# Performance work log

Measured on AMD Instinct MI355X. Metric: run time of the kernel, lower is better.

## Reference

```python
import jax, jax.numpy as jnp
import numpy as np

B, N, M = 8, 4096, 77
Q_DIM, CTX_DIM = 1024, 768
H, D = 16, 64
INNER = H * D  # 1024


def setup_inputs() -> dict:
    key = jax.random.key(0)
    ks = jax.random.split(key, 7)
    x = jax.random.normal(ks[0], (B, N, Q_DIM), dtype=jnp.float32)
    context = jax.random.normal(ks[1], (B, M, CTX_DIM), dtype=jnp.float32)
    # Linear weights stored as [in, out] so y = x @ W (no bias for q/k/v).
    Wq = jax.random.normal(ks[2], (Q_DIM, INNER), dtype=jnp.float32) * (Q_DIM ** -0.5)
    Wk = jax.random.normal(ks[3], (CTX_DIM, INNER), dtype=jnp.float32) * (CTX_DIM ** -0.5)
    Wv = jax.random.normal(ks[4], (CTX_DIM, INNER), dtype=jnp.float32) * (CTX_DIM ** -0.5)
    Wo = jax.random.normal(ks[5], (INNER, Q_DIM), dtype=jnp.float32) * (INNER ** -0.5)
    bo = jax.random.normal(ks[6], (Q_DIM,), dtype=jnp.float32) * 0.01
    return {"x": x, "context": context, "Wq": Wq, "Wk": Wk, "Wv": Wv, "Wo": Wo, "bo": bo}


def reference(x, context, Wq, Wk, Wv, Wo, bo):
    scale = D ** -0.5
    # Project and split heads: [B, S, H*D] -> [B, H, S, D]
    def heads(t):
        b, s, _ = t.shape
        return t.reshape(b, s, H, D).transpose(0, 2, 1, 3)
    q = heads(x @ Wq)        # [B, H, N, D]
    k = heads(context @ Wk)  # [B, H, M, D]
    v = heads(context @ Wv)  # [B, H, M, D]
    scores = jnp.einsum('bhid,bhjd->bhij', q, k) * scale  # [B, H, N, M]
    attn = jax.nn.softmax(scores, axis=-1)
    out = jnp.einsum('bhij,bhjd->bhid', attn, v)          # [B, H, N, D]
    out = out.transpose(0, 2, 1, 3).reshape(x.shape[0], x.shape[1], INNER)
    return out @ Wo + bo  # dropout p=0.0 -> identity
```

## Files before the change

kernel.cpp:

```cpp
#include <hip/hip_runtime.h>
#include <hip/hip_bf16.h>

typedef _Float16 f16x8 __attribute__((ext_vector_type(8)));
typedef float f32x4 __attribute__((ext_vector_type(4)));

#define MFMA16(a, b, c) __builtin_amdgcn_mfma_f32_16x16x32_f16(a, b, c, 0, 0, 0)

__device__ __forceinline__ void load_lds16(const void* g, void* l) {
  __builtin_amdgcn_global_load_lds(
      (__attribute__((address_space(1))) void*)g,
      (__attribute__((address_space(3))) void*)l, 16, 0, 0);
}

__global__ __launch_bounds__(256) void k_prep(const float* __restrict__ x,
                                              const float* __restrict__ ctx,
                                              const float* __restrict__ Wq,
                                              const float* __restrict__ Wk,
                                              const float* __restrict__ Wv,
                                              const float* __restrict__ Wo,
                                              _Float16* __restrict__ xh,
                                              _Float16* __restrict__ ctxh,
                                              _Float16* __restrict__ Wqt,
                                              _Float16* __restrict__ Wkt,
                                              _Float16* __restrict__ Wvt,
                                              _Float16* __restrict__ Wot,
                                              _Float16* __restrict__ Vtg) {
  __shared__ float tile[64][65];
  const int b = blockIdx.x, t = threadIdx.x;

  if (b < 4096) {
    for (int i = b * 256 + t; i < 4194304; i += 4096 * 256) {
      const float4* p = (const float4*)(x + (size_t)i * 8);
      float4 a = p[0], c = p[1];
      f16x8 v = {(_Float16)a.x, (_Float16)a.y, (_Float16)a.z, (_Float16)a.w,
                 (_Float16)c.x, (_Float16)c.y, (_Float16)c.z, (_Float16)c.w};
      *(f16x8*)(xh + (size_t)i * 8) = v;
    }
    return;
  }
  if (b < 4327) {
    int i = (b - 4096) * 256 + t;
    const float4* p = (const float4*)(ctx + (size_t)i * 8);
    float4 a = p[0], c = p[1];
    f16x8 v = {(_Float16)a.x, (_Float16)a.y, (_Float16)a.z, (_Float16)a.w,
               (_Float16)c.x, (_Float16)c.y, (_Float16)c.z, (_Float16)c.w};
    *(f16x8*)(ctxh + (size_t)i * 8) = v;
    return;
  }
  if (b >= 5223) {
    int i = (b - 5223) * 256 + t;
    ((f16x8*)Vtg)[i] = f16x8{};
    return;
  }
  const float* tin;
  _Float16* tout;
  int TK, TN, i;
  if (b < 4583)      { tin = Wq; tout = Wqt; TK = 1024; TN = 1024; i = b - 4327; }
  else if (b < 4775) { tin = Wk; tout = Wkt; TK = 768;  TN = 1024; i = b - 4583; }
  else if (b < 4967) { tin = Wv; tout = Wvt; TK = 768;  TN = 1024; i = b - 4775; }
  else               { tin = Wo; tout = Wot; TK = 1024; TN = 1024; i = b - 4967; }
  int n0 = (i & 15) * 64, k0 = (i >> 4) * 64;
  {
    int nn = t & 63, kb = t >> 6;
#pragma unroll
    for (int s = 0; s < 16; ++s) {
      int kk = kb + s * 4;
      tile[kk][nn] = tin[(size_t)(k0 + kk) * TN + n0 + nn];
    }
  }
  __syncthreads();
  {
    int kk = t & 63, nb = t >> 6;
#pragma unroll
    for (int s = 0; s < 16; ++s) {
      int nn = nb + s * 4;
      tout[(size_t)(n0 + nn) * TK + k0 + kk] = (_Float16)tile[kk][nn];
    }
  }
}

__global__ __launch_bounds__(64) void k_kvproj(const _Float16* __restrict__ ctxh,
                                               const _Float16* __restrict__ Wkt,
                                               const _Float16* __restrict__ Wvt,
                                               _Float16* __restrict__ Kg,
                                               _Float16* __restrict__ Vtg) {
  int mt = blockIdx.x, nt = blockIdx.y;
  int lane = threadIdx.x;
  int l15 = lane & 15, lhi = lane >> 4;
  int arow = mt * 16 + l15;
  if (arow > 615) arow = 615;
  const _Float16* ap = ctxh + (size_t)arow * 768 + lhi * 8;
  const _Float16* kp = Wkt + (size_t)(nt * 16 + l15) * 768 + lhi * 8;
  const _Float16* vp = Wvt + (size_t)(nt * 16 + l15) * 768 + lhi * 8;
  f32x4 ak = {0.f, 0.f, 0.f, 0.f}, av = {0.f, 0.f, 0.f, 0.f};
#pragma unroll 4
  for (int ks = 0; ks < 24; ++ks) {
    f16x8 a = *(const f16x8*)(ap + ks * 32);
    f16x8 bk = *(const f16x8*)(kp + ks * 32);
    f16x8 bv = *(const f16x8*)(vp + ks * 32);
    ak = MFMA16(a, bk, ak);
    av = MFMA16(a, bv, av);
  }
  int n = nt * 16 + l15, h = n >> 6, d = n & 63;
#pragma unroll
  for (int j = 0; j < 4; ++j) {
    int gm = mt * 16 + lhi * 4 + j;
    if (gm < 616) {
      int b = gm / 77, m = gm - b * 77;
      Kg[((size_t)(b * 16 + h) * 77 + m) * 64 + d] = (_Float16)ak[j];
      Vtg[((size_t)(b * 16 + h) * 64 + d) * 128 + m] = (_Float16)av[j];
    }
  }
}

template <int MODE>
__global__ __launch_bounds__(512, 2) void k_gemm9(const _Float16* __restrict__ A,
                                                  const _Float16* __restrict__ Bt,
                                                  void* __restrict__ Cout,
                                                  const float* __restrict__ bias,
                                                  const _Float16* __restrict__ Kg,
                                                  const _Float16* __restrict__ Vtg,
                                                  int M, int N, int K) {
  __shared__ __align__(16) char lds[MODE == 0 ? 163840 : 131072];
  const int t = threadIdx.x, wid = t >> 6, lane = t & 63;
  const int wr = wid >> 2, wc = wid & 3;
  const int l15 = lane & 15, lhi = lane >> 4;

  int nwg = gridDim.x, bid = blockIdx.x;
  int wg = ((nwg & 7) == 0) ? ((bid & 7) * (nwg >> 3) + (bid >> 3)) : bid;
  const int nTN = N >> 8;
  const int tm = wg / nTN, tn = wg % nTN;

  const _Float16* Ag = A + (size_t)tm * 256 * K;
  const _Float16* Bg = Bt + (size_t)tn * 256 * K;
  const size_t stg = (size_t)(wid * 8 + (lane >> 3)) * K +
                     (size_t)(((lane & 7) ^ ((lane >> 3) & 7)) * 8);
  const int dstg = wid * 1024;

  const int x7 = l15 & 7;
  const int cs0 = (lhi ^ x7) << 4;
  const int cs1 = ((4 + lhi) ^ x7) << 4;
  const int aoff = wr * 16384 + l15 * 128;
  const int boff = 32768 + wc * 8192 + l15 * 128;

  f32x4 acc[8][4];
#pragma unroll
  for (int i = 0; i < 8; ++i)
#pragma unroll
    for (int j = 0; j < 4; ++j) acc[i][j] = f32x4{0.f, 0.f, 0.f, 0.f};
  f16x8 a0k0[4], a0k1[4], a1k0[4], a1k1[4];
  f16x8 b00[2], b01[2], b10[2], b11[2];

#define STG_A(T, RB) load_lds16(Ag + stg + (size_t)(RB) * K + (T) * 64, \
                                lds + ((T) & 1) * 65536 + (RB) * 128 + dstg)
#define STG_B(T, RB) load_lds16(Bg + stg + (size_t)(RB) * K + (T) * 64, \
                                lds + ((T) & 1) * 65536 + 32768 + (RB) * 128 + dstg)
#define STG_TILE(T) { STG_A(T, 0); STG_A(T, 64); STG_A(T, 128); STG_A(T, 192);  \
                      STG_B(T, 0); STG_B(T, 64); STG_B(T, 128); STG_B(T, 192); }
#define RDA(DST, BUF, MH, CS) { const int p_ = (BUF) * 65536 + aoff + (MH) * 8192; \
    _Pragma("unroll") for (int mf = 0; mf < 4; ++mf)                               \
      DST[mf] = *(const f16x8*)&lds[p_ + mf * 2048 + (CS)]; }
#define RDB(DST, BUF, NH, CS) { const int q_ = (BUF) * 65536 + boff + (NH) * 4096; \
    _Pragma("unroll") for (int nf = 0; nf < 2; ++nf)                               \
      DST[nf] = *(const f16x8*)&lds[q_ + nf * 2048 + (CS)]; }
#define MMC(MH, NH, AR, BR) { __builtin_amdgcn_s_setprio(1);                       \
    _Pragma("unroll") for (int mf = 0; mf < 4; ++mf)                               \
      _Pragma("unroll") for (int nf = 0; nf < 2; ++nf)                             \
        acc[(MH)*4+mf][(NH)*2+nf] = MFMA16(AR[mf], BR[nf],                         \
                                           acc[(MH)*4+mf][(NH)*2+nf]);             \
    __builtin_amdgcn_s_setprio(0); }
#define VM0 asm volatile("s_waitcnt vmcnt(0)" ::: "memory")
#define BAR __builtin_amdgcn_s_barrier()

#define TILE(BUF, T, STG_ON)                                                       \
  {                                                                                \
    VM0; BAR;                                                                      \
    RDA(a0k0, BUF, 0, cs0); RDB(b00, BUF, 0, cs0);                                 \
    RDB(b10, BUF, 1, cs0);                                                         \
    if (STG_ON) STG_TILE((T) + 1);                                                 \
    MMC(0, 0, a0k0, b00);                                                          \
    RDA(a1k0, BUF, 1, cs0); MMC(0, 1, a0k0, b10);                                  \
    RDA(a1k1, BUF, 1, cs1); MMC(1, 1, a1k0, b10);                                  \
    RDB(b01, BUF, 0, cs1);  MMC(1, 0, a1k0, b00);                                  \
    RDB(b11, BUF, 1, cs1);  MMC(1, 0, a1k1, b01);                                  \
    RDA(a0k1, BUF, 0, cs1); MMC(1, 1, a1k1, b11);                                  \
    MMC(0, 1, a0k1, b11);                                                          \
    MMC(0, 0, a0k1, b01);                                                          \
  }

  const int nT = K >> 6;

  STG_TILE(0);

  for (int i = 0; i < (nT >> 1) - 1; ++i) {
    TILE(0, 2 * i, true);
    TILE(1, 2 * i + 1, true);
  }
  TILE(0, nT - 2, true);
  TILE(1, nT - 1, false);

  if (MODE == 1) {
    const long rbase = (long)tm * 256 + wr * 128;
    const int cbase = tn * 256 + wc * 64;
#pragma unroll
    for (int mf = 0; mf < 8; ++mf)
#pragma unroll
      for (int nf = 0; nf < 4; ++nf) {
        int c = cbase + nf * 16 + l15;
        float bv = bias[c];
#pragma unroll
        for (int j = 0; j < 4; ++j) {
          long r = rbase + mf * 16 + lhi * 4 + j;
          ((float*)Cout)[r * N + c] = acc[mf][nf][j] + bv;
        }
      }
    return;
  }

  BAR;

  const int h = tn * 4 + wc;
  const int bh = (tm >> 4) * 16 + h;
  const _Float16* Kgp = Kg + (size_t)bh * (77 * 64);
  const _Float16* Vgp = Vtg + (size_t)bh * (64 * 128);

  const int qbase = wid * 16384;
#pragma unroll
  for (int mf = 0; mf < 8; ++mf)
#pragma unroll
    for (int nf = 0; nf < 4; ++nf)
#pragma unroll
      for (int j = 0; j < 4; ++j) {
        int row = mf * 16 + lhi * 4 + j;
        int d = nf * 16 + l15;
        int by = (row * 128 + d * 2) ^ ((row & 7) << 4);
        *(_Float16*)&lds[qbase + by] = (_Float16)acc[mf][nf][j];
      }

  const int pbase = 131072 + wid * 4096;
#pragma unroll
  for (int i = 0; i < 4; ++i)
    *(f16x8*)&lds[pbase + lane * 64 + i * 16] = f16x8{};

  f16x8 kf[5][2];
#pragma unroll
  for (int ct = 0; ct < 5; ++ct) {
    int m = ct * 16 + l15;
    kf[ct][0] = *(const f16x8*)(Kgp + m * 64 + lhi * 8);
    kf[ct][1] = *(const f16x8*)(Kgp + m * 64 + 32 + lhi * 8);
  }
  f16x8 vf[3][4];
#pragma unroll
  for (int ks = 0; ks < 3; ++ks)
#pragma unroll
    for (int dt = 0; dt < 4; ++dt) {
      int d = dt * 16 + l15;
      vf[ks][dt] = *(const f16x8*)(Vgp + d * 128 + ks * 32 + lhi * 8);
    }

  const long orow0 = (long)tm * 256 + wr * 128;
  _Float16* aOut = (_Float16*)Cout;

  for (int mf = 0; mf < 8; ++mf) {
    const int qm = qbase + mf * 2048 + l15 * 128;
    f16x8 q0 = *(const f16x8*)&lds[qm + cs0];
    f16x8 q1 = *(const f16x8*)&lds[qm + cs1];

    float e[5][4];
    float mx[4] = {-1e30f, -1e30f, -1e30f, -1e30f};
#pragma unroll
    for (int ct = 0; ct < 5; ++ct) {
      f32x4 s = {0.f, 0.f, 0.f, 0.f};
      s = MFMA16(q0, kf[ct][0], s);
      s = MFMA16(q1, kf[ct][1], s);
      bool valid = (ct * 16 + l15) < 77;
#pragma unroll
      for (int j = 0; j < 4; ++j) {
        float v = valid ? s[j] * 0.125f : -1e30f;
        e[ct][j] = v;
        mx[j] = fmaxf(mx[j], v);
      }
    }
#pragma unroll
    for (int off = 1; off < 16; off <<= 1)
#pragma unroll
      for (int j = 0; j < 4; ++j) mx[j] = fmaxf(mx[j], __shfl_xor(mx[j], off, 64));
    float sm[4] = {0.f, 0.f, 0.f, 0.f};
#pragma unroll
    for (int ct = 0; ct < 5; ++ct)
#pragma unroll
      for (int j = 0; j < 4; ++j) {
        float ev = __expf(e[ct][j] - mx[j]);
        e[ct][j] = ev;
        sm[j] += ev;
      }
#pragma unroll
    for (int off = 1; off < 16; off <<= 1)
#pragma unroll
      for (int j = 0; j < 4; ++j) sm[j] += __shfl_xor(sm[j], off, 64);
    float rs[4];
#pragma unroll
    for (int j = 0; j < 4; ++j) rs[j] = 1.0f / sm[j];

#pragma unroll
    for (int ct = 0; ct < 5; ++ct) {
      int m = ct * 16 + l15;
#pragma unroll
      for (int j = 0; j < 4; ++j) {
        int r = lhi * 4 + j;
        *(_Float16*)&lds[pbase + ((r * 256 + m * 2) ^ ((r & 7) << 4))] =
            (_Float16)(e[ct][j] * rs[j]);
      }
    }

    f32x4 o[4] = {{0.f,0.f,0.f,0.f},{0.f,0.f,0.f,0.f},{0.f,0.f,0.f,0.f},{0.f,0.f,0.f,0.f}};
#pragma unroll
    for (int ks = 0; ks < 3; ++ks) {
      int m0b = ks * 64 + lhi * 16;
      f16x8 pa = *(const f16x8*)&lds[pbase + ((l15 * 256 + m0b) ^ ((l15 & 7) << 4))];
#pragma unroll
      for (int dt = 0; dt < 4; ++dt)
        o[dt] = MFMA16(pa, vf[ks][dt], o[dt]);
    }
    _Float16* op = aOut + (size_t)(orow0 + mf * 16 + lhi * 4) * 1024 + h * 64;
#pragma unroll
    for (int dt = 0; dt < 4; ++dt)
#pragma unroll
      for (int j = 0; j < 4; ++j)
        op[(size_t)j * 1024 + dt * 16 + l15] = (_Float16)o[dt][j];
  }
#undef STG_A
#undef STG_B
#undef STG_TILE
#undef RDA
#undef RDB
#undef MMC
#undef TILE
#undef VM0
#undef BAR
}

extern "C" void kernel_launch(void* const* d_in, const int* in_sizes, int n_in,
                              void* d_out, int out_size, void* d_ws, size_t ws_size,
                              hipStream_t stream) {
  const float* x   = (const float*)d_in[0];
  const float* ctx = (const float*)d_in[1];
  const float* Wq  = (const float*)d_in[2];
  const float* Wk  = (const float*)d_in[3];
  const float* Wv  = (const float*)d_in[4];
  const float* Wo  = (const float*)d_in[5];
  const float* bo  = (const float*)d_in[6];

  char* ws = (char*)d_ws;
  _Float16* xh   = (_Float16*)(ws + 0);
  _Float16* Wqt  = (_Float16*)(ws + 67108864);
  _Float16* Wkt  = (_Float16*)(ws + 69206016);
  _Float16* Wvt  = (_Float16*)(ws + 70778880);
  _Float16* Wot  = (_Float16*)(ws + 72351744);
  _Float16* ctxh = (_Float16*)(ws + 74448896);
  _Float16* Kg   = (_Float16*)(ws + 75395072);
  _Float16* Vtg  = (_Float16*)(ws + 76656640);
  _Float16* aOut = (_Float16*)(ws + 78774272);

  k_prep<<<5735, 256, 0, stream>>>(x, ctx, Wq, Wk, Wv, Wo,
                                   xh, ctxh, Wqt, Wkt, Wvt, Wot, Vtg);
  k_kvproj<<<dim3(39, 64), 64, 0, stream>>>(ctxh, Wkt, Wvt, Kg, Vtg);
  k_gemm9<0><<<dim3(512), dim3(512), 0, stream>>>(xh, Wqt, (void*)aOut, nullptr,
                                                  Kg, Vtg, 32768, 1024, 1024);
  k_gemm9<1><<<dim3(512), dim3(512), 0, stream>>>(aOut, Wot, d_out, bo,
                                                  nullptr, nullptr, 32768, 1024, 1024);
}
```

Measured before the change: 244.1 us.

## Fuse fp32-to-fp16 conversion of x into the Q-projection GEMM A-tile loads

Removes the separate pass that converted x to fp16 in the prep kernel and instead loads fp32 x directly inside the first GEMM, converting in registers and writing fp16 into LDS. This eliminates a full write and re-read of an fp16 copy of x. In exchange, the GEMM reads fp32 A (twice the bytes per tile, repeated across N tiles), uses extra registers for staging, and adds LDS write and waits to the pipelined loop.

```diff
diff --git a/kernel.cpp b/kernel.cpp
--- a/kernel.cpp
+++ b/kernel.cpp
@@ -12,13 +12,11 @@
       (__attribute__((address_space(3))) void*)l, 16, 0, 0);
 }
 
-__global__ __launch_bounds__(256) void k_prep(const float* __restrict__ x,
-                                              const float* __restrict__ ctx,
+__global__ __launch_bounds__(256) void k_prep(const float* __restrict__ ctx,
                                               const float* __restrict__ Wq,
                                               const float* __restrict__ Wk,
                                               const float* __restrict__ Wv,
                                               const float* __restrict__ Wo,
-                                              _Float16* __restrict__ xh,
                                               _Float16* __restrict__ ctxh,
                                               _Float16* __restrict__ Wqt,
                                               _Float16* __restrict__ Wkt,
@@ -28,18 +26,8 @@
   __shared__ float tile[64][65];
   const int b = blockIdx.x, t = threadIdx.x;
 
-  if (b < 4096) {
-    for (int i = b * 256 + t; i < 4194304; i += 4096 * 256) {
-      const float4* p = (const float4*)(x + (size_t)i * 8);
-      float4 a = p[0], c = p[1];
-      f16x8 v = {(_Float16)a.x, (_Float16)a.y, (_Float16)a.z, (_Float16)a.w,
-                 (_Float16)c.x, (_Float16)c.y, (_Float16)c.z, (_Float16)c.w};
-      *(f16x8*)(xh + (size_t)i * 8) = v;
-    }
-    return;
-  }
-  if (b < 4327) {
-    int i = (b - 4096) * 256 + t;
+  if (b < 231) {
+    int i = b * 256 + t;
     const float4* p = (const float4*)(ctx + (size_t)i * 8);
     float4 a = p[0], c = p[1];
     f16x8 v = {(_Float16)a.x, (_Float16)a.y, (_Float16)a.z, (_Float16)a.w,
@@ -47,18 +35,18 @@
     *(f16x8*)(ctxh + (size_t)i * 8) = v;
     return;
   }
-  if (b >= 5223) {
-    int i = (b - 5223) * 256 + t;
+  if (b >= 1127) {
+    int i = (b - 1127) * 256 + t;
     ((f16x8*)Vtg)[i] = f16x8{};
     return;
   }
   const float* tin;
   _Float16* tout;
   int TK, TN, i;
-  if (b < 4583)      { tin = Wq; tout = Wqt; TK = 1024; TN = 1024; i = b - 4327; }
-  else if (b < 4775) { tin = Wk; tout = Wkt; TK = 768;  TN = 1024; i = b - 4583; }
-  else if (b < 4967) { tin = Wv; tout = Wvt; TK = 768;  TN = 1024; i = b - 4775; }
-  else               { tin = Wo; tout = Wot; TK = 1024; TN = 1024; i = b - 4967; }
+  if (b < 487)      { tin = Wq; tout = Wqt; TK = 1024; TN = 1024; i = b - 231; }
+  else if (b < 679) { tin = Wk; tout = Wkt; TK = 768;  TN = 1024; i = b - 487; }
+  else if (b < 871) { tin = Wv; tout = Wvt; TK = 768;  TN = 1024; i = b - 679; }
+  else              { tin = Wo; tout = Wot; TK = 1024; TN = 1024; i = b - 871; }
   int n0 = (i & 15) * 64, k0 = (i >> 4) * 64;
   {
     int nn = t & 63, kb = t >> 6;
@@ -115,6 +103,7 @@
 
 template <int MODE>
 __global__ __launch_bounds__(512, 2) void k_gemm9(const _Float16* __restrict__ A,
+                                                  const float* __restrict__ Axf,
                                                   const _Float16* __restrict__ Bt,
                                                   void* __restrict__ Cout,
                                                   const float* __restrict__ bias,
@@ -136,6 +125,9 @@
   const size_t stg = (size_t)(wid * 8 + (lane >> 3)) * K +
                      (size_t)(((lane & 7) ^ ((lane >> 3) & 7)) * 8);
   const int dstg = wid * 1024;
+  const float* Axp = Axf + (size_t)(tm * 256 + wid * 8 + (lane >> 3)) * K +
+                     (size_t)(((lane & 7) ^ ((lane >> 3) & 7)) * 8);
+  const int awr = dstg + lane * 16;
 
   const int x7 = l15 & 7;
   const int cs0 = (lhi ^ x7) << 4;
@@ -150,13 +142,20 @@
     for (int j = 0; j < 4; ++j) acc[i][j] = f32x4{0.f, 0.f, 0.f, 0.f};
   f16x8 a0k0[4], a0k1[4], a1k0[4], a1k1[4];
   f16x8 b00[2], b01[2], b10[2], b11[2];
+  float4 ar0[4], ar1[4];
 
 #define STG_A(T, RB) load_lds16(Ag + stg + (size_t)(RB) * K + (T) * 64, \
                                 lds + ((T) & 1) * 65536 + (RB) * 128 + dstg)
 #define STG_B(T, RB) load_lds16(Bg + stg + (size_t)(RB) * K + (T) * 64, \
                                 lds + ((T) & 1) * 65536 + 32768 + (RB) * 128 + dstg)
-#define STG_TILE(T) { STG_A(T, 0); STG_A(T, 64); STG_A(T, 128); STG_A(T, 192);  \
-                      STG_B(T, 0); STG_B(T, 64); STG_B(T, 128); STG_B(T, 192); }
+#define LD_A32(T) { _Pragma("unroll") for (int s = 0; s < 4; ++s) {                \
+      const float* sp_ = Axp + (size_t)s * 64 * K + (T) * 64;                      \
+      ar0[s] = *(const float4*)sp_; ar1[s] = *(const float4*)(sp_ + 4); } }
+#define WR_A(T) { _Pragma("unroll") for (int s = 0; s < 4; ++s) {                  \
+      f16x8 v_ = {(_Float16)ar0[s].x, (_Float16)ar0[s].y, (_Float16)ar0[s].z,      \
+                  (_Float16)ar0[s].w, (_Float16)ar1[s].x, (_Float16)ar1[s].y,      \
+                  (_Float16)ar1[s].z, (_Float16)ar1[s].w};                         \
+      *(f16x8*)&lds[((T) & 1) * 65536 + s * 8192 + awr] = v_; } }
 #define RDA(DST, BUF, MH, CS) { const int p_ = (BUF) * 65536 + aoff + (MH) * 8192; \
     _Pragma("unroll") for (int mf = 0; mf < 4; ++mf)                               \
       DST[mf] = *(const f16x8*)&lds[p_ + mf * 2048 + (CS)]; }
@@ -170,14 +169,17 @@
                                            acc[(MH)*4+mf][(NH)*2+nf]);             \
     __builtin_amdgcn_s_setprio(0); }
 #define VM0 asm volatile("s_waitcnt vmcnt(0)" ::: "memory")
+#define VMLG0 asm volatile("s_waitcnt vmcnt(0) lgkmcnt(0)" ::: "memory")
 #define BAR __builtin_amdgcn_s_barrier()
 
-#define TILE(BUF, T, STG_ON)                                                       \
+#define TILE1(BUF, T, STG_ON)                                                      \
   {                                                                                \
     VM0; BAR;                                                                      \
     RDA(a0k0, BUF, 0, cs0); RDB(b00, BUF, 0, cs0);                                 \
     RDB(b10, BUF, 1, cs0);                                                         \
-    if (STG_ON) STG_TILE((T) + 1);                                                 \
+    if (STG_ON) { STG_A((T) + 1, 0); STG_A((T) + 1, 64); STG_A((T) + 1, 128);      \
+                  STG_A((T) + 1, 192); STG_B((T) + 1, 0); STG_B((T) + 1, 64);      \
+                  STG_B((T) + 1, 128); STG_B((T) + 1, 192); }                      \
     MMC(0, 0, a0k0, b00);                                                          \
     RDA(a1k0, BUF, 1, cs0); MMC(0, 1, a0k0, b10);                                  \
     RDA(a1k1, BUF, 1, cs1); MMC(1, 1, a1k0, b10);                                  \
@@ -187,17 +189,48 @@
     MMC(0, 1, a0k1, b11);                                                          \
     MMC(0, 0, a0k1, b01);                                                          \
   }
+#define TILE0(BUF, T, STG_ON)                                                      \
+  {                                                                                \
+    VMLG0; BAR;                                                                    \
+    RDA(a0k0, BUF, 0, cs0); RDB(b00, BUF, 0, cs0);                                 \
+    RDB(b10, BUF, 1, cs0);                                                         \
+    if (STG_ON) { LD_A32((T) + 1); STG_B((T) + 1, 0); STG_B((T) + 1, 64);          \
+                  STG_B((T) + 1, 128); STG_B((T) + 1, 192); }                      \
+    MMC(0, 0, a0k0, b00);                                                          \
+    RDA(a1k0, BUF, 1, cs0); MMC(0, 1, a0k0, b10);                                  \
+    RDA(a1k1, BUF, 1, cs1); MMC(1, 1, a1k0, b10);                                  \
+    RDB(b01, BUF, 0, cs1);  MMC(1, 0, a1k0, b00);                                  \
+    RDB(b11, BUF, 1, cs1);  MMC(1, 0, a1k1, b01);                                  \
+    RDA(a0k1, BUF, 0, cs1); MMC(1, 1, a1k1, b11);                                  \
+    if (STG_ON) WR_A((T) + 1);                                                     \
+    MMC(0, 1, a0k1, b11);                                                          \
+    MMC(0, 0, a0k1, b01);                                                          \
+  }
 
   const int nT = K >> 6;
 
-  STG_TILE(0);
-
-  for (int i = 0; i < (nT >> 1) - 1; ++i) {
-    TILE(0, 2 * i, true);
-    TILE(1, 2 * i + 1, true);
-  }
-  TILE(0, nT - 2, true);
-  TILE(1, nT - 1, false);
+  if (MODE == 0) {
+    LD_A32(0);
+    STG_B(0, 0); STG_B(0, 64); STG_B(0, 128); STG_B(0, 192);
+    WR_A(0);
+    VMLG0; BAR;
+    for (int i = 0; i < (nT >> 1) - 1; ++i) {
+      TILE0(0, 2 * i, true);
+      TILE0(1, 2 * i + 1, true);
+    }
+    TILE0(0, nT - 2, true);
+    TILE0(1, nT - 1, false);
+  } else {
+    STG_A(0, 0); STG_A(0, 64); STG_A(0, 128); STG_A(0, 192);
+    STG_B(0, 0); STG_B(0, 64); STG_B(0, 128); STG_B(0, 192);
+    VM0; BAR;
+    for (int i = 0; i < (nT >> 1) - 1; ++i) {
+      TILE1(0, 2 * i, true);
+      TILE1(1, 2 * i + 1, true);
+    }
+    TILE1(0, nT - 2, true);
+    TILE1(1, nT - 1, false);
+  }
 
   if (MODE == 1) {
     const long rbase = (long)tm * 256 + wr * 128;
@@ -331,12 +364,15 @@
   }
 #undef STG_A
 #undef STG_B
-#undef STG_TILE
+#undef LD_A32
+#undef WR_A
 #undef RDA
 #undef RDB
 #undef MMC
-#undef TILE
+#undef TILE0
+#undef TILE1
 #undef VM0
+#undef VMLG0
 #undef BAR
 }
 
@@ -352,7 +388,6 @@
   const float* bo  = (const float*)d_in[6];
 
   char* ws = (char*)d_ws;
-  _Float16* xh   = (_Float16*)(ws + 0);
   _Float16* Wqt  = (_Float16*)(ws + 67108864);
   _Float16* Wkt  = (_Float16*)(ws + 69206016);
   _Float16* Wvt  = (_Float16*)(ws + 70778880);
@@ -362,11 +397,11 @@
   _Float16* Vtg  = (_Float16*)(ws + 76656640);
   _Float16* aOut = (_Float16*)(ws + 78774272);
 
-  k_prep<<<5735, 256, 0, stream>>>(x, ctx, Wq, Wk, Wv, Wo,
-                                   xh, ctxh, Wqt, Wkt, Wvt, Wot, Vtg);
+  k_prep<<<1639, 256, 0, stream>>>(ctx, Wq, Wk, Wv, Wo,
+                                   ctxh, Wqt, Wkt, Wvt, Wot, Vtg);
   k_kvproj<<<dim3(39, 64), 64, 0, stream>>>(ctxh, Wkt, Wvt, Kg, Vtg);
-  k_gemm9<0><<<dim3(512), dim3(512), 0, stream>>>(xh, Wqt, (void*)aOut, nullptr,
-                                                  Kg, Vtg, 32768, 1024, 1024);
-  k_gemm9<1><<<dim3(512), dim3(512), 0, stream>>>(aOut, Wot, d_out, bo,
+  k_gemm9<0><<<dim3(512), dim3(512), 0, stream>>>(nullptr, x, Wqt, (void*)aOut,
+                                                  nullptr, Kg, Vtg, 32768, 1024, 1024);
+  k_gemm9<1><<<dim3(512), dim3(512), 0, stream>>>(aOut, nullptr, Wot, d_out, bo,
                                                   nullptr, nullptr, 32768, 1024, 1024);
 }
```

Measured after the change: 265.3 us. 8.7% more time.
